# Performance work log

Hardware: AMD Instinct MI355X
Metric: run time of the kernel (lower is better)

The kernel has to match this reference:

```python
import jax, jax.numpy as jnp
import numpy as np

N = 100000      # num nodes
R = 32          # num relations
E = 3200000     # num edges
F_IN = 128      # feat_len
H = 16          # hidden dim (hard-coded in source)
C = 8           # num classes


def setup_inputs() -> dict:
    key = jax.random.key(0)
    k1, k2, k3, k4, k5 = jax.random.split(key, 5)
    emb = jax.random.normal(k1, (N, F_IN), dtype=jnp.float32)
    W1 = jax.random.normal(k2, (R, F_IN, H), dtype=jnp.float32) * 0.05
    W2 = jax.random.normal(k3, (R, H, C), dtype=jnp.float32) * 0.05
    edge_index = jax.random.randint(k4, (2, E), 0, N, dtype=jnp.int64)
    edge_type = jax.random.randint(k5, (E,), 0, R, dtype=jnp.int64)
    return {"emb": emb, "W1": W1, "W2": W2,
            "edge_index": edge_index, "edge_type": edge_type}


def _rgcn_layer(x, W, src, dst, etype, edge_norm):
    # x: [N, Fin], W: [R, Fin, Fout]
    # Transform once per relation, then gather per edge (avoids [E,Fin,Fout]).
    xw = jnp.einsum('nf,rfo->rno', x, W)          # [R, N, Fout]
    msg = xw[etype, src] * edge_norm[:, None]      # [E, Fout]
    return jax.ops.segment_sum(msg, dst, num_segments=N)  # [N, Fout]


def reference(emb, W1, W2, edge_index, edge_type):
    src, dst = edge_index[0], edge_index[1]
    # PyG RGCNConv aggr='mean': normalize by per-(dst, relation) in-degree.
    key_idx = dst * R + edge_type                              # [E]
    deg = jax.ops.segment_sum(jnp.ones((E,), emb.dtype), key_idx,
                              num_segments=N * R)              # [N*R]
    edge_norm = 1.0 / jnp.maximum(deg, 1.0)
    edge_norm = edge_norm[key_idx]                             # [E]

    h = jax.nn.relu(_rgcn_layer(emb, W1, src, dst, edge_type, edge_norm))
    h = _rgcn_layer(h, W2, src, dst, edge_type, edge_norm)
    return jax.nn.log_softmax(h, axis=1)
```

## Files before the change

### kernel.cpp

```cpp
#include <hip/hip_runtime.h>
#include <hip/hip_bf16.h>
#include <math.h>

#define N_NODES 100000
#define R 32
#define E_EDGES 3200000
#define F_IN 128
#define HDIM 16
#define CDIM 8
#define NOUT 512
#define M_PAD 100032
#define NBUCK 391
#define KEYS 8192
#define P1CHUNK 8192
#define P1GRID ((E_EDGES + P1CHUNK - 1) / P1CHUNK)

typedef __attribute__((ext_vector_type(8))) short bf16x8;
typedef __attribute__((ext_vector_type(4))) float f32x4;
typedef __attribute__((ext_vector_type(2))) _Float16 f16x2;

static __device__ __forceinline__ unsigned short f2bf(float f) {
    unsigned int u = __float_as_uint(f);
    unsigned int r = (u + 0x7FFFu + ((u >> 16) & 1u)) >> 16;
    return (unsigned short)r;
}
static __device__ __forceinline__ f16x2 asf16x2(float f) {
    union { float f; f16x2 h; } u; u.f = f; return u.h;
}

#if __has_builtin(__builtin_amdgcn_fdot2)
static __device__ __forceinline__ float FDOT2(f16x2 a, f16x2 b, float c) {
    return __builtin_amdgcn_fdot2(a, b, c, false);
}
#else
static __device__ __forceinline__ float FDOT2(f16x2 a, f16x2 b, float c) {
    return c + (float)a.x * (float)b.x + (float)a.y * (float)b.y;
}
#endif

__global__ __launch_bounds__(512) void k_hist(const int* __restrict__ dst,
                                              int* __restrict__ bucketcount) {
    __shared__ int h[NBUCK];
    int t = threadIdx.x;
    for (int j = t; j < NBUCK; j += 512) h[j] = 0;
    __syncthreads();
    int e0 = blockIdx.x * P1CHUNK;
    int e1 = e0 + P1CHUNK; if (e1 > E_EDGES) e1 = E_EDGES;
    int n4 = (e1 - e0) >> 2;
    const int4* d4 = (const int4*)(dst + e0);
    for (int i = t; i < n4; i += 512) {
        int4 v = d4[i];
        atomicAdd(&h[v.x >> 8], 1);
        atomicAdd(&h[v.y >> 8], 1);
        atomicAdd(&h[v.z >> 8], 1);
        atomicAdd(&h[v.w >> 8], 1);
    }
    __syncthreads();
    for (int j = t; j < NBUCK; j += 512)
        if (h[j]) atomicAdd(&bucketcount[j], h[j]);
}

__global__ __launch_bounds__(512) void k_scanb(const int* __restrict__ bucketcount,
                                               int* __restrict__ bucketstart,
                                               int* __restrict__ gcursor,
                                               int* __restrict__ rowstart) {
    __shared__ int sb[NBUCK + 1];
    int t = threadIdx.x;
    if (t == 0) {
        int acc = 0;
        for (int b = 0; b < NBUCK; ++b) { int v = bucketcount[b]; sb[b] = acc; acc += v; }
        sb[NBUCK] = acc;
        rowstart[N_NODES] = acc;
    }
    __syncthreads();
    for (int j = t; j <= NBUCK; j += 512) bucketstart[j] = sb[j];
    for (int j = t; j < NBUCK; j += 512) gcursor[j] = sb[j];
}

__global__ __launch_bounds__(512) void k_bucket(const int* __restrict__ src,
                                                const int* __restrict__ dst,
                                                const int* __restrict__ et,
                                                int* __restrict__ gcursor,
                                                unsigned int* __restrict__ ebuf) {
    __shared__ int hist[NBUCK];
    __shared__ int rank[NBUCK];
    __shared__ int base[NBUCK];
    int t = threadIdx.x;
    for (int j = t; j < NBUCK; j += 512) { hist[j] = 0; rank[j] = 0; }
    __syncthreads();
    int e0 = blockIdx.x * P1CHUNK;
    int e1 = e0 + P1CHUNK; if (e1 > E_EDGES) e1 = E_EDGES;
    int n4 = (e1 - e0) >> 2;
    const int4* d4 = (const int4*)(dst + e0);
    const int4* s4 = (const int4*)(src + e0);
    const int4* t4 = (const int4*)(et + e0);
    for (int i = t; i < n4; i += 512) {
        int4 v = d4[i];
        atomicAdd(&hist[v.x >> 8], 1);
        atomicAdd(&hist[v.y >> 8], 1);
        atomicAdd(&hist[v.z >> 8], 1);
        atomicAdd(&hist[v.w >> 8], 1);
    }
    __syncthreads();
    for (int j = t; j < NBUCK; j += 512)
        base[j] = hist[j] ? atomicAdd(&gcursor[j], hist[j]) : 0;
    __syncthreads();
    for (int i = t; i < n4; i += 512) {
        int4 dv = d4[i];
        int4 sv = s4[i];
        int4 tv = t4[i];
        int ds[4] = {dv.x, dv.y, dv.z, dv.w};
        int ss[4] = {sv.x, sv.y, sv.z, sv.w};
        int ts[4] = {tv.x, tv.y, tv.z, tv.w};
        #pragma unroll
        for (int u = 0; u < 4; ++u) {
            int d = ds[u];
            int bk = d >> 8;
            unsigned pk = ((unsigned)(d & 255) << 22) | ((unsigned)ts[u] << 17)
                        | (unsigned)ss[u];
            int lr = atomicAdd(&rank[bk], 1);
            ebuf[base[bk] + lr] = pk;
        }
    }
}

__global__ __launch_bounds__(1024) void k_sortb(const unsigned int* __restrict__ ebuf,
                                                const int* __restrict__ bucketstart,
                                                int* __restrict__ rowstart,
                                                unsigned int* __restrict__ elist) {
    __shared__ unsigned int cnt[KEYS];
    __shared__ int wsum[16];
    int t = threadIdx.x, b = blockIdx.x;
    int e0 = bucketstart[b], e1 = bucketstart[b + 1];
    #pragma unroll
    for (int j = 0; j < KEYS / 1024; ++j) cnt[t + j * 1024] = 0;
    __syncthreads();
    for (int i = e0 + t; i < e1; i += 1024)
        atomicAdd(&cnt[ebuf[i] >> 17], 1u);
    __syncthreads();
    int kbase = t * (KEYS / 1024);
    int s = 0;
    #pragma unroll
    for (int j = 0; j < KEYS / 1024; ++j) s += (int)cnt[kbase + j];
    int lane = t & 63, wv = t >> 6;
    int sc = s;
    #pragma unroll
    for (int off = 1; off < 64; off <<= 1) {
        int v = __shfl_up(sc, off, 64);
        if (lane >= off) sc += v;
    }
    if (lane == 63) wsum[wv] = sc;
    __syncthreads();
    if (t < 16) {
        int v = wsum[t];
        int sc2 = v;
        #pragma unroll
        for (int off = 1; off < 16; off <<= 1) {
            int u = __shfl_up(sc2, off, 16);
            if (t >= off) sc2 += u;
        }
        wsum[t] = sc2 - v;
    }
    __syncthreads();
    int run = wsum[wv] + sc - s;
    #pragma unroll
    for (int j = 0; j < KEYS / 1024; ++j) {
        unsigned v = cnt[kbase + j];
        unsigned lc = v > 1023u ? 1023u : v;
        cnt[kbase + j] = (unsigned)run | (lc << 20);
        run += (int)v;
    }
    __syncthreads();
    if (t < 256) {
        int d = b * 256 + t;
        if (d < N_NODES) rowstart[d] = e0 + (int)(cnt[t * 32] & 0xFFFFFu);
    }
    __syncthreads();
    for (int i = e0 + t; i < e1; i += 1024) {
        unsigned pk = ebuf[i];
        int key = pk >> 17;
        unsigned vv = atomicAdd(&cnt[key], 1u);
        int pos = (int)(vv & 0xFFFFFu);
        unsigned len = (vv >> 20) & 1023u;
        elist[e0 + pos] = (pk & 0x3FFFFFu) | (len << 22);
    }
}

__global__ __launch_bounds__(256) void k_cvt(const float* __restrict__ emb,
                                             unsigned short* __restrict__ out) {
    int g = blockIdx.x * 256 + threadIdx.x;
    size_t base = (size_t)g * 4;
    if (base >= (size_t)M_PAD * F_IN) return;
    int row = (int)(base >> 7);
    ushort4 o;
    if (row < N_NODES) {
        float4 a = *(const float4*)(emb + base);
        o.x = f2bf(a.x); o.y = f2bf(a.y); o.z = f2bf(a.z); o.w = f2bf(a.w);
    } else {
        o.x = o.y = o.z = o.w = 0;
    }
    *(ushort4*)(out + base) = o;
}

__global__ __launch_bounds__(256) void k_prep_w(const float* __restrict__ W1,
                                                unsigned short* __restrict__ BmT) {
    int i = blockIdx.x * 256 + threadIdx.x;
    if (i >= NOUT * F_IN) return;
    int n = i >> 7;
    int f = i & 127;
    int r = n >> 4;
    int o = n & 15;
    BmT[i] = f2bf(W1[r * (F_IN * HDIM) + f * HDIM + o]);
}

__global__ __launch_bounds__(256) void k_gemm(const unsigned short* __restrict__ Abf,
                                              const unsigned short* __restrict__ BmT,
                                              unsigned short* __restrict__ C) {
    __shared__ unsigned short As[64 * 136];
    __shared__ unsigned short Bs[128 * 136];
    int t = threadIdx.x;
    int row0 = blockIdx.x * 64;
    int col0 = blockIdx.y * 128;

    #pragma unroll
    for (int j = 0; j < 4; ++j) {
        int idx = t + j * 256;
        int r = idx >> 4;
        int u = idx & 15;
        float4 v = *(const float4*)(Abf + (size_t)(row0 + r) * F_IN + u * 8);
        *(float4*)(&As[r * 136 + u * 8]) = v;
    }
    #pragma unroll
    for (int j = 0; j < 8; ++j) {
        int idx = t + j * 256;
        int r = idx >> 4;
        int u = idx & 15;
        float4 v = *(const float4*)(BmT + (size_t)(col0 + r) * F_IN + u * 8);
        *(float4*)(&Bs[r * 136 + u * 8]) = v;
    }
    __syncthreads();

    int w = t >> 6;
    int lane = t & 63;
    int q = lane >> 4;
    int mr = lane & 15;

    f32x4 acc[8] = {};
    const unsigned short* ap = &As[(w * 16 + mr) * 136 + q * 8];
    #pragma unroll
    for (int kk = 0; kk < 4; ++kk) {
        bf16x8 af = *(const bf16x8*)(ap + kk * 32);
        #pragma unroll
        for (int tt = 0; tt < 8; ++tt) {
            bf16x8 bf = *(const bf16x8*)(&Bs[(tt * 16 + mr) * 136 + q * 8 + kk * 32]);
            acc[tt] = __builtin_amdgcn_mfma_f32_16x16x32_bf16(af, bf, acc[tt], 0, 0, 0);
        }
    }
    #pragma unroll
    for (int tt = 0; tt < 8; ++tt) {
        #pragma unroll
        for (int j = 0; j < 4; ++j) {
            int row = row0 + w * 16 + q * 4 + j;
            C[(size_t)row * NOUT + col0 + tt * 16 + mr] = f2bf(acc[tt][j]);
        }
    }
}

__global__ __launch_bounds__(256) void k_gather1(const int* __restrict__ rowstart,
                                                 const unsigned int* __restrict__ elist,
                                                 const unsigned short* __restrict__ xw1,
                                                 _Float16* __restrict__ h) {
    __shared__ float nlut[1024];
    int t = threadIdx.x;
    for (int j = t; j < 1024; j += 256) nlut[j] = 1.0f / (float)(j ? j : 1);
    __syncthreads();
    int g = t >> 3;
    int c = t & 7;
    int d = blockIdx.x * 32 + g;
    if (d >= N_NODES) return;
    int i = rowstart[d], end = rowstart[d + 1];
    float a0 = 0.f, a1 = 0.f, b0 = 0.f, b1 = 0.f;
    for (; i + 1 < end; i += 2) {
        unsigned pk0 = elist[i];
        unsigned pk1 = elist[i + 1];
        int s0 = pk0 & 0x1FFFF, s1 = pk1 & 0x1FFFF;
        int r0 = (pk0 >> 17) & 31, r1 = (pk1 >> 17) & 31;
        float nm0 = nlut[pk0 >> 22], nm1 = nlut[pk1 >> 22];
        unsigned x0 = *(const unsigned*)(xw1 + (size_t)s0 * NOUT + r0 * HDIM + c * 2);
        unsigned x1 = *(const unsigned*)(xw1 + (size_t)s1 * NOUT + r1 * HDIM + c * 2);
        a0 += __uint_as_float(x0 << 16) * nm0;
        a1 += __uint_as_float(x0 & 0xFFFF0000u) * nm0;
        b0 += __uint_as_float(x1 << 16) * nm1;
        b1 += __uint_as_float(x1 & 0xFFFF0000u) * nm1;
    }
    if (i < end) {
        unsigned pk = elist[i];
        int s = pk & 0x1FFFF;
        int r = (pk >> 17) & 31;
        float nm = nlut[pk >> 22];
        unsigned x = *(const unsigned*)(xw1 + (size_t)s * NOUT + r * HDIM + c * 2);
        a0 += __uint_as_float(x << 16) * nm;
        a1 += __uint_as_float(x & 0xFFFF0000u) * nm;
    }
    f16x2 o;
    o.x = (_Float16)fmaxf(a0 + b0, 0.f);
    o.y = (_Float16)fmaxf(a1 + b1, 0.f);
    *(f16x2*)(h + (size_t)d * HDIM + c * 2) = o;
}

#define W2P 260
__global__ __launch_bounds__(256) void k_gather2(const int* __restrict__ rowstart,
                                                 const unsigned int* __restrict__ elist,
                                                 const _Float16* __restrict__ h,
                                                 const float* __restrict__ W2,
                                                 float* __restrict__ out) {
    __shared__ f16x2 sW2h[CDIM * W2P];
    __shared__ float nlut[1024];
    int t = threadIdx.x;
    for (int j = t; j < 1024; j += 256) nlut[j] = 1.0f / (float)(j ? j : 1);
    #pragma unroll
    for (int j = 0; j < 8; ++j) {
        int idx = t + j * 256;
        int c = idx >> 8;
        int rem = idx & 255;
        int r = rem >> 3;
        int jj = rem & 7;
        f16x2 p;
        p.x = (_Float16)W2[r * (HDIM * CDIM) + (2 * jj) * CDIM + c];
        p.y = (_Float16)W2[r * (HDIM * CDIM) + (2 * jj + 1) * CDIM + c];
        sW2h[c * W2P + rem] = p;
    }
    __syncthreads();

    int g = t >> 3;
    int c = t & 7;
    int d = blockIdx.x * 32 + g;
    if (d >= N_NODES) return;
    const f16x2* wc = &sW2h[c * W2P];
    int i = rowstart[d], end = rowstart[d + 1];
    float acc0 = 0.f, acc1 = 0.f;
    for (; i + 1 < end; i += 2) {
        unsigned pk0 = elist[i];
        unsigned pk1 = elist[i + 1];
        int s0 = pk0 & 0x1FFFF, s1 = pk1 & 0x1FFFF;
        int r0 = (pk0 >> 17) & 31, r1 = (pk1 >> 17) & 31;
        float nm0 = nlut[pk0 >> 22], nm1 = nlut[pk1 >> 22];
        const float4* hp0 = (const float4*)(h + (size_t)s0 * HDIM);
        const float4* hp1 = (const float4*)(h + (size_t)s1 * HDIM);
        float4 u0 = hp0[0], u1 = hp0[1];
        float4 v0 = hp1[0], v1 = hp1[1];
        const f16x2* wp0 = wc + r0 * 8;
        const f16x2* wp1 = wc + r1 * 8;
        float sd0 = 0.f, sd1 = 0.f;
        sd0 = FDOT2(asf16x2(u0.x), wp0[0], sd0);
        sd0 = FDOT2(asf16x2(u0.y), wp0[1], sd0);
        sd0 = FDOT2(asf16x2(u0.z), wp0[2], sd0);
        sd0 = FDOT2(asf16x2(u0.w), wp0[3], sd0);
        sd0 = FDOT2(asf16x2(u1.x), wp0[4], sd0);
        sd0 = FDOT2(asf16x2(u1.y), wp0[5], sd0);
        sd0 = FDOT2(asf16x2(u1.z), wp0[6], sd0);
        sd0 = FDOT2(asf16x2(u1.w), wp0[7], sd0);
        sd1 = FDOT2(asf16x2(v0.x), wp1[0], sd1);
        sd1 = FDOT2(asf16x2(v0.y), wp1[1], sd1);
        sd1 = FDOT2(asf16x2(v0.z), wp1[2], sd1);
        sd1 = FDOT2(asf16x2(v0.w), wp1[3], sd1);
        sd1 = FDOT2(asf16x2(v1.x), wp1[4], sd1);
        sd1 = FDOT2(asf16x2(v1.y), wp1[5], sd1);
        sd1 = FDOT2(asf16x2(v1.z), wp1[6], sd1);
        sd1 = FDOT2(asf16x2(v1.w), wp1[7], sd1);
        acc0 += nm0 * sd0;
        acc1 += nm1 * sd1;
    }
    if (i < end) {
        unsigned pk = elist[i];
        int s = pk & 0x1FFFF;
        int r = (pk >> 17) & 31;
        float nm = nlut[pk >> 22];
        const float4* hp = (const float4*)(h + (size_t)s * HDIM);
        float4 u0 = hp[0], u1 = hp[1];
        const f16x2* wp = wc + r * 8;
        float sd = 0.f;
        sd = FDOT2(asf16x2(u0.x), wp[0], sd);
        sd = FDOT2(asf16x2(u0.y), wp[1], sd);
        sd = FDOT2(asf16x2(u0.z), wp[2], sd);
        sd = FDOT2(asf16x2(u0.w), wp[3], sd);
        sd = FDOT2(asf16x2(u1.x), wp[4], sd);
        sd = FDOT2(asf16x2(u1.y), wp[5], sd);
        sd = FDOT2(asf16x2(u1.z), wp[6], sd);
        sd = FDOT2(asf16x2(u1.w), wp[7], sd);
        acc0 += nm * sd;
    }
    float acc = acc0 + acc1;
    float m = acc;
    #pragma unroll
    for (int mask = 1; mask < 8; mask <<= 1)
        m = fmaxf(m, __shfl_xor(m, mask, 8));
    float ex = expf(acc - m);
    float ssumv = ex;
    #pragma unroll
    for (int mask = 1; mask < 8; mask <<= 1)
        ssumv += __shfl_xor(ssumv, mask, 8);
    out[(size_t)d * CDIM + c] = acc - m - logf(ssumv);
}

extern "C" void kernel_launch(void* const* d_in, const int* in_sizes, int n_in,
                              void* d_out, int out_size, void* d_ws, size_t ws_size,
                              hipStream_t stream) {
    const float* emb = (const float*)d_in[0];
    const float* W1  = (const float*)d_in[1];
    const float* W2  = (const float*)d_in[2];
    const int* ei    = (const int*)d_in[3];
    const int* et    = (const int*)d_in[4];
    const int* srcp  = ei;
    const int* dstp  = ei + E_EDGES;

    char* ws = (char*)d_ws;
    size_t off = 0;
    #define ALIGN256(x) (((x) + 255) & ~(size_t)255)
    int* bucketcount = (int*)(ws + off); off = ALIGN256(off + 512 * 4);
    int* bucketstart = (int*)(ws + off); off = ALIGN256(off + 512 * 4);
    int* gcursor     = (int*)(ws + off); off = ALIGN256(off + 512 * 4);
    int* rowstart    = (int*)(ws + off); off = ALIGN256(off + ((size_t)N_NODES + 8) * 4);
    unsigned int* ebuf  = (unsigned int*)(ws + off); off = ALIGN256(off + (size_t)E_EDGES * 4);
    unsigned int* elist = (unsigned int*)(ws + off); off = ALIGN256(off + (size_t)E_EDGES * 4);
    unsigned short* BmT  = (unsigned short*)(ws + off); off = ALIGN256(off + (size_t)NOUT * F_IN * 2);
    unsigned short* ebf  = (unsigned short*)(ws + off); off = ALIGN256(off + (size_t)M_PAD * F_IN * 2);
    unsigned short* xw1  = (unsigned short*)(ws + off); off = ALIGN256(off + (size_t)M_PAD * NOUT * 2);
    _Float16* h          = (_Float16*)(ws + off);       off = ALIGN256(off + (size_t)N_NODES * HDIM * 2);
    float* out = (float*)d_out;

    hipMemsetAsync(bucketcount, 0, NBUCK * 4, stream);

    k_hist<<<P1GRID, 512, 0, stream>>>(dstp, bucketcount);
    k_scanb<<<1, 512, 0, stream>>>(bucketcount, bucketstart, gcursor, rowstart);
    k_bucket<<<P1GRID, 512, 0, stream>>>(srcp, dstp, et, gcursor, ebuf);
    k_sortb<<<NBUCK, 1024, 0, stream>>>(ebuf, bucketstart, rowstart, elist);

    k_cvt<<<((M_PAD * F_IN / 4) + 255) / 256, 256, 0, stream>>>(emb, ebf);
    k_prep_w<<<(NOUT * F_IN) / 256, 256, 0, stream>>>(W1, BmT);
    dim3 g_gemm(M_PAD / 64, NOUT / 128);
    k_gemm<<<g_gemm, 256, 0, stream>>>(ebf, BmT, xw1);

    k_gather1<<<(N_NODES + 31) / 32, 256, 0, stream>>>(rowstart, elist, xw1, h);
    k_gather2<<<(N_NODES + 31) / 32, 256, 0, stream>>>(rowstart, elist, h, W2, out);
}
```

Baseline: 347.4 us.

## Merge preprocessing kernels via fixed-capacity buckets and widen gather1 per-thread loads

Bucketing now writes into fixed-capacity per-bucket slots (CAP 9216), so the separate histogram pass is gone. Bucketing, the bf16 conversion of emb and the W1 repack now run as one heterogeneous launch, and the per-bucket sort runs alongside the GEMM in a second combined launch, cutting launch count and the serialisation between them. gather1 now has each thread handle 4 features with 8-byte loads and unroll by 4 edges. The cost is a larger workspace, and results will be wrong if a bucket ever holds more than CAP edges. The combined kernels also force both roles to share one block size and one shared-memory allocation.

```diff
diff --git a/kernel.cpp b/kernel.cpp
--- a/kernel.cpp
+++ b/kernel.cpp
@@ -11,19 +11,31 @@
 #define NOUT 512
 #define M_PAD 100032
 #define NBUCK 391
+#define CAP 9216
 #define KEYS 8192
 #define P1CHUNK 8192
-#define P1GRID ((E_EDGES + P1CHUNK - 1) / P1CHUNK)
+#define CVT_BLKS 6252
+#define PREP_BLKS 128
+#define FRONT_GRID (NBUCK + CVT_BLKS + PREP_BLKS)
+#define GEMM_BLKS 6252
+#define MID_GRID (NBUCK + GEMM_BLKS)
 
 typedef __attribute__((ext_vector_type(8))) short bf16x8;
 typedef __attribute__((ext_vector_type(4))) float f32x4;
 typedef __attribute__((ext_vector_type(2))) _Float16 f16x2;
+typedef __attribute__((ext_vector_type(4))) _Float16 f16x4;
 
 static __device__ __forceinline__ unsigned short f2bf(float f) {
     unsigned int u = __float_as_uint(f);
     unsigned int r = (u + 0x7FFFu + ((u >> 16) & 1u)) >> 16;
     return (unsigned short)r;
 }
+static __device__ __forceinline__ float bfl(unsigned x) {
+    return __uint_as_float(x << 16);
+}
+static __device__ __forceinline__ float bfh(unsigned x) {
+    return __uint_as_float(x & 0xFFFF0000u);
+}
 static __device__ __forceinline__ f16x2 asf16x2(float f) {
     union { float f; f16x2 h; } u; u.f = f; return u.h;
 }
@@ -38,230 +50,201 @@
 }
 #endif
 
-__global__ __launch_bounds__(512) void k_hist(const int* __restrict__ dst,
-                                              int* __restrict__ bucketcount) {
-    __shared__ int h[NBUCK];
-    int t = threadIdx.x;
-    for (int j = t; j < NBUCK; j += 512) h[j] = 0;
-    __syncthreads();
-    int e0 = blockIdx.x * P1CHUNK;
-    int e1 = e0 + P1CHUNK; if (e1 > E_EDGES) e1 = E_EDGES;
-    int n4 = (e1 - e0) >> 2;
-    const int4* d4 = (const int4*)(dst + e0);
-    for (int i = t; i < n4; i += 512) {
-        int4 v = d4[i];
-        atomicAdd(&h[v.x >> 8], 1);
-        atomicAdd(&h[v.y >> 8], 1);
-        atomicAdd(&h[v.z >> 8], 1);
-        atomicAdd(&h[v.w >> 8], 1);
-    }
-    __syncthreads();
-    for (int j = t; j < NBUCK; j += 512)
-        if (h[j]) atomicAdd(&bucketcount[j], h[j]);
-}
-
-__global__ __launch_bounds__(512) void k_scanb(const int* __restrict__ bucketcount,
+__global__ __launch_bounds__(512) void k_front(const int* __restrict__ src,
+                                               const int* __restrict__ dst,
+                                               const int* __restrict__ et,
+                                               const float* __restrict__ emb,
+                                               const float* __restrict__ W1,
+                                               int* __restrict__ gcursor,
+                                               unsigned int* __restrict__ ebuf,
+                                               unsigned short* __restrict__ ebf,
+                                               unsigned short* __restrict__ BmT) {
+    __shared__ int sh[3 * NBUCK];
+    int b = blockIdx.x, t = threadIdx.x;
+    if (b < NBUCK) {
+        int* hist = sh;
+        int* rank = sh + NBUCK;
+        int* base = sh + 2 * NBUCK;
+        for (int j = t; j < NBUCK; j += 512) { hist[j] = 0; rank[j] = 0; }
+        __syncthreads();
+        int e0 = b * P1CHUNK;
+        int e1 = e0 + P1CHUNK; if (e1 > E_EDGES) e1 = E_EDGES;
+        int n4 = (e1 - e0) >> 2;
+        const int4* d4 = (const int4*)(dst + e0);
+        const int4* s4 = (const int4*)(src + e0);
+        const int4* t4 = (const int4*)(et + e0);
+        for (int i = t; i < n4; i += 512) {
+            int4 v = d4[i];
+            atomicAdd(&hist[v.x >> 8], 1);
+            atomicAdd(&hist[v.y >> 8], 1);
+            atomicAdd(&hist[v.z >> 8], 1);
+            atomicAdd(&hist[v.w >> 8], 1);
+        }
+        __syncthreads();
+        for (int j = t; j < NBUCK; j += 512)
+            base[j] = hist[j] ? atomicAdd(&gcursor[j], hist[j]) : 0;
+        __syncthreads();
+        for (int i = t; i < n4; i += 512) {
+            int4 dv = d4[i];
+            int4 sv = s4[i];
+            int4 tv = t4[i];
+            int ds[4] = {dv.x, dv.y, dv.z, dv.w};
+            int ss[4] = {sv.x, sv.y, sv.z, sv.w};
+            int ts[4] = {tv.x, tv.y, tv.z, tv.w};
+            #pragma unroll
+            for (int u = 0; u < 4; ++u) {
+                int d = ds[u];
+                int bk = d >> 8;
+                unsigned pk = ((unsigned)(d & 255) << 22) | ((unsigned)ts[u] << 17)
+                            | (unsigned)ss[u];
+                int lr = atomicAdd(&rank[bk], 1);
+                ebuf[(size_t)bk * CAP + base[bk] + lr] = pk;
+            }
+        }
+    } else if (b < NBUCK + CVT_BLKS) {
+        size_t base = ((size_t)(b - NBUCK) * 512 + t) * 4;
+        int row = (int)(base >> 7);
+        ushort4 o;
+        if (row < N_NODES) {
+            float4 a = *(const float4*)(emb + base);
+            o.x = f2bf(a.x); o.y = f2bf(a.y); o.z = f2bf(a.z); o.w = f2bf(a.w);
+        } else {
+            o.x = o.y = o.z = o.w = 0;
+        }
+        *(ushort4*)(ebf + base) = o;
+    } else {
+        int i = (b - NBUCK - CVT_BLKS) * 512 + t;
+        int n = i >> 7;
+        int f = i & 127;
+        int r = n >> 4;
+        int o = n & 15;
+        BmT[i] = f2bf(W1[r * (F_IN * HDIM) + f * HDIM + o]);
+    }
+}
+
+__global__ __launch_bounds__(512) void k_scanb(const int* __restrict__ gcursor,
                                                int* __restrict__ bucketstart,
-                                               int* __restrict__ gcursor,
                                                int* __restrict__ rowstart) {
     __shared__ int sb[NBUCK + 1];
     int t = threadIdx.x;
     if (t == 0) {
         int acc = 0;
-        for (int b = 0; b < NBUCK; ++b) { int v = bucketcount[b]; sb[b] = acc; acc += v; }
+        for (int b = 0; b < NBUCK; ++b) { int v = gcursor[b]; sb[b] = acc; acc += v; }
         sb[NBUCK] = acc;
         rowstart[N_NODES] = acc;
     }
     __syncthreads();
     for (int j = t; j <= NBUCK; j += 512) bucketstart[j] = sb[j];
-    for (int j = t; j < NBUCK; j += 512) gcursor[j] = sb[j];
-}
-
-__global__ __launch_bounds__(512) void k_bucket(const int* __restrict__ src,
-                                                const int* __restrict__ dst,
-                                                const int* __restrict__ et,
-                                                int* __restrict__ gcursor,
-                                                unsigned int* __restrict__ ebuf) {
-    __shared__ int hist[NBUCK];
-    __shared__ int rank[NBUCK];
-    __shared__ int base[NBUCK];
-    int t = threadIdx.x;
-    for (int j = t; j < NBUCK; j += 512) { hist[j] = 0; rank[j] = 0; }
-    __syncthreads();
-    int e0 = blockIdx.x * P1CHUNK;
-    int e1 = e0 + P1CHUNK; if (e1 > E_EDGES) e1 = E_EDGES;
-    int n4 = (e1 - e0) >> 2;
-    const int4* d4 = (const int4*)(dst + e0);
-    const int4* s4 = (const int4*)(src + e0);
-    const int4* t4 = (const int4*)(et + e0);
-    for (int i = t; i < n4; i += 512) {
-        int4 v = d4[i];
-        atomicAdd(&hist[v.x >> 8], 1);
-        atomicAdd(&hist[v.y >> 8], 1);
-        atomicAdd(&hist[v.z >> 8], 1);
-        atomicAdd(&hist[v.w >> 8], 1);
-    }
-    __syncthreads();
-    for (int j = t; j < NBUCK; j += 512)
-        base[j] = hist[j] ? atomicAdd(&gcursor[j], hist[j]) : 0;
-    __syncthreads();
-    for (int i = t; i < n4; i += 512) {
-        int4 dv = d4[i];
-        int4 sv = s4[i];
-        int4 tv = t4[i];
-        int ds[4] = {dv.x, dv.y, dv.z, dv.w};
-        int ss[4] = {sv.x, sv.y, sv.z, sv.w};
-        int ts[4] = {tv.x, tv.y, tv.z, tv.w};
-        #pragma unroll
-        for (int u = 0; u < 4; ++u) {
-            int d = ds[u];
-            int bk = d >> 8;
-            unsigned pk = ((unsigned)(d & 255) << 22) | ((unsigned)ts[u] << 17)
-                        | (unsigned)ss[u];
-            int lr = atomicAdd(&rank[bk], 1);
-            ebuf[base[bk] + lr] = pk;
-        }
-    }
-}
-
-__global__ __launch_bounds__(1024) void k_sortb(const unsigned int* __restrict__ ebuf,
-                                                const int* __restrict__ bucketstart,
-                                                int* __restrict__ rowstart,
-                                                unsigned int* __restrict__ elist) {
-    __shared__ unsigned int cnt[KEYS];
-    __shared__ int wsum[16];
-    int t = threadIdx.x, b = blockIdx.x;
-    int e0 = bucketstart[b], e1 = bucketstart[b + 1];
-    #pragma unroll
-    for (int j = 0; j < KEYS / 1024; ++j) cnt[t + j * 1024] = 0;
-    __syncthreads();
-    for (int i = e0 + t; i < e1; i += 1024)
-        atomicAdd(&cnt[ebuf[i] >> 17], 1u);
-    __syncthreads();
-    int kbase = t * (KEYS / 1024);
-    int s = 0;
-    #pragma unroll
-    for (int j = 0; j < KEYS / 1024; ++j) s += (int)cnt[kbase + j];
-    int lane = t & 63, wv = t >> 6;
-    int sc = s;
-    #pragma unroll
-    for (int off = 1; off < 64; off <<= 1) {
-        int v = __shfl_up(sc, off, 64);
-        if (lane >= off) sc += v;
-    }
-    if (lane == 63) wsum[wv] = sc;
-    __syncthreads();
-    if (t < 16) {
-        int v = wsum[t];
-        int sc2 = v;
-        #pragma unroll
-        for (int off = 1; off < 16; off <<= 1) {
-            int u = __shfl_up(sc2, off, 16);
-            if (t >= off) sc2 += u;
-        }
-        wsum[t] = sc2 - v;
-    }
-    __syncthreads();
-    int run = wsum[wv] + sc - s;
-    #pragma unroll
-    for (int j = 0; j < KEYS / 1024; ++j) {
-        unsigned v = cnt[kbase + j];
-        unsigned lc = v > 1023u ? 1023u : v;
-        cnt[kbase + j] = (unsigned)run | (lc << 20);
-        run += (int)v;
-    }
-    __syncthreads();
-    if (t < 256) {
-        int d = b * 256 + t;
-        if (d < N_NODES) rowstart[d] = e0 + (int)(cnt[t * 32] & 0xFFFFFu);
-    }
-    __syncthreads();
-    for (int i = e0 + t; i < e1; i += 1024) {
-        unsigned pk = ebuf[i];
-        int key = pk >> 17;
-        unsigned vv = atomicAdd(&cnt[key], 1u);
-        int pos = (int)(vv & 0xFFFFFu);
-        unsigned len = (vv >> 20) & 1023u;
-        elist[e0 + pos] = (pk & 0x3FFFFFu) | (len << 22);
-    }
-}
-
-__global__ __launch_bounds__(256) void k_cvt(const float* __restrict__ emb,
-                                             unsigned short* __restrict__ out) {
-    int g = blockIdx.x * 256 + threadIdx.x;
-    size_t base = (size_t)g * 4;
-    if (base >= (size_t)M_PAD * F_IN) return;
-    int row = (int)(base >> 7);
-    ushort4 o;
-    if (row < N_NODES) {
-        float4 a = *(const float4*)(emb + base);
-        o.x = f2bf(a.x); o.y = f2bf(a.y); o.z = f2bf(a.z); o.w = f2bf(a.w);
+}
+
+__global__ __launch_bounds__(256) void k_mid(const unsigned int* __restrict__ ebuf,
+                                             const int* __restrict__ gcursor,
+                                             const int* __restrict__ bucketstart,
+                                             int* __restrict__ rowstart,
+                                             unsigned int* __restrict__ elist,
+                                             const unsigned short* __restrict__ Abf,
+                                             const unsigned short* __restrict__ BmT,
+                                             unsigned short* __restrict__ C) {
+    __shared__ __align__(16) char smem[52224 + 64];
+    int b = blockIdx.x, t = threadIdx.x;
+    if (b < NBUCK) {
+        unsigned int* cnt = (unsigned int*)smem;
+        int* wsum = (int*)(smem + 32768);
+        int cntE = gcursor[b];
+        size_t esrc = (size_t)b * CAP;
+        int e0 = bucketstart[b];
+        #pragma unroll
+        for (int j = 0; j < KEYS / 256; ++j) cnt[t + j * 256] = 0;
+        __syncthreads();
+        for (int i = t; i < cntE; i += 256)
+            atomicAdd(&cnt[ebuf[esrc + i] >> 17], 1u);
+        __syncthreads();
+        int kbase = t * (KEYS / 256);
+        int s = 0;
+        #pragma unroll
+        for (int j = 0; j < KEYS / 256; ++j) s += (int)cnt[kbase + j];
+        int lane = t & 63, wv = t >> 6;
+        int sc = s;
+        #pragma unroll
+        for (int off = 1; off < 64; off <<= 1) {
+            int v = __shfl_up(sc, off, 64);
+            if (lane >= off) sc += v;
+        }
+        if (lane == 63) wsum[wv] = sc;
+        __syncthreads();
+        if (t == 0) {
+            int a = 0;
+            #pragma unroll
+            for (int w = 0; w < 4; ++w) { int v = wsum[w]; wsum[w] = a; a += v; }
+        }
+        __syncthreads();
+        int run = wsum[wv] + sc - s;
+        #pragma unroll
+        for (int j = 0; j < KEYS / 256; ++j) {
+            unsigned v = cnt[kbase + j];
+            unsigned lc = v > 1023u ? 1023u : v;
+            cnt[kbase + j] = (unsigned)run | (lc << 20);
+            run += (int)v;
+        }
+        __syncthreads();
+        {
+            int d = b * 256 + t;
+            if (d < N_NODES) rowstart[d] = e0 + (int)(cnt[t * 32] & 0xFFFFFu);
+        }
+        __syncthreads();
+        for (int i = t; i < cntE; i += 256) {
+            unsigned pk = ebuf[esrc + i];
+            int key = pk >> 17;
+            unsigned vv = atomicAdd(&cnt[key], 1u);
+            int pos = (int)(vv & 0xFFFFFu);
+            unsigned len = (vv >> 20) & 1023u;
+            elist[e0 + pos] = (pk & 0x3FFFFFu) | (len << 22);
+        }
     } else {
-        o.x = o.y = o.z = o.w = 0;
-    }
-    *(ushort4*)(out + base) = o;
-}
-
-__global__ __launch_bounds__(256) void k_prep_w(const float* __restrict__ W1,
-                                                unsigned short* __restrict__ BmT) {
-    int i = blockIdx.x * 256 + threadIdx.x;
-    if (i >= NOUT * F_IN) return;
-    int n = i >> 7;
-    int f = i & 127;
-    int r = n >> 4;
-    int o = n & 15;
-    BmT[i] = f2bf(W1[r * (F_IN * HDIM) + f * HDIM + o]);
-}
-
-__global__ __launch_bounds__(256) void k_gemm(const unsigned short* __restrict__ Abf,
-                                              const unsigned short* __restrict__ BmT,
-                                              unsigned short* __restrict__ C) {
-    __shared__ unsigned short As[64 * 136];
-    __shared__ unsigned short Bs[128 * 136];
-    int t = threadIdx.x;
-    int row0 = blockIdx.x * 64;
-    int col0 = blockIdx.y * 128;
-
-    #pragma unroll
-    for (int j = 0; j < 4; ++j) {
-        int idx = t + j * 256;
-        int r = idx >> 4;
-        int u = idx & 15;
-        float4 v = *(const float4*)(Abf + (size_t)(row0 + r) * F_IN + u * 8);
-        *(float4*)(&As[r * 136 + u * 8]) = v;
-    }
-    #pragma unroll
-    for (int j = 0; j < 8; ++j) {
-        int idx = t + j * 256;
-        int r = idx >> 4;
-        int u = idx & 15;
-        float4 v = *(const float4*)(BmT + (size_t)(col0 + r) * F_IN + u * 8);
-        *(float4*)(&Bs[r * 136 + u * 8]) = v;
-    }
-    __syncthreads();
-
-    int w = t >> 6;
-    int lane = t & 63;
-    int q = lane >> 4;
-    int mr = lane & 15;
-
-    f32x4 acc[8] = {};
-    const unsigned short* ap = &As[(w * 16 + mr) * 136 + q * 8];
-    #pragma unroll
-    for (int kk = 0; kk < 4; ++kk) {
-        bf16x8 af = *(const bf16x8*)(ap + kk * 32);
+        unsigned short* As = (unsigned short*)smem;
+        unsigned short* Bs = (unsigned short*)(smem + 17408);
+        int bb = b - NBUCK;
+        int row0 = (bb >> 2) * 64;
+        int col0 = (bb & 3) * 128;
+        #pragma unroll
+        for (int j = 0; j < 4; ++j) {
+            int idx = t + j * 256;
+            int r = idx >> 4;
+            int u = idx & 15;
+            float4 v = *(const float4*)(Abf + (size_t)(row0 + r) * F_IN + u * 8);
+            *(float4*)(&As[r * 136 + u * 8]) = v;
+        }
+        #pragma unroll
+        for (int j = 0; j < 8; ++j) {
+            int idx = t + j * 256;
+            int r = idx >> 4;
+            int u = idx & 15;
+            float4 v = *(const float4*)(BmT + (size_t)(col0 + r) * F_IN + u * 8);
+            *(float4*)(&Bs[r * 136 + u * 8]) = v;
+        }
+        __syncthreads();
+        int w = t >> 6;
+        int lane = t & 63;
+        int q = lane >> 4;
+        int mr = lane & 15;
+        f32x4 acc[8] = {};
+        const unsigned short* ap = &As[(w * 16 + mr) * 136 + q * 8];
+        #pragma unroll
+        for (int kk = 0; kk < 4; ++kk) {
+            bf16x8 af = *(const bf16x8*)(ap + kk * 32);
+            #pragma unroll
+            for (int tt = 0; tt < 8; ++tt) {
+                bf16x8 bf = *(const bf16x8*)(&Bs[(tt * 16 + mr) * 136 + q * 8 + kk * 32]);
+                acc[tt] = __builtin_amdgcn_mfma_f32_16x16x32_bf16(af, bf, acc[tt], 0, 0, 0);
+            }
+        }
         #pragma unroll
         for (int tt = 0; tt < 8; ++tt) {
-            bf16x8 bf = *(const bf16x8*)(&Bs[(tt * 16 + mr) * 136 + q * 8 + kk * 32]);
-            acc[tt] = __builtin_amdgcn_mfma_f32_16x16x32_bf16(af, bf, acc[tt], 0, 0, 0);
-        }
-    }
-    #pragma unroll
-    for (int tt = 0; tt < 8; ++tt) {
-        #pragma unroll
-        for (int j = 0; j < 4; ++j) {
-            int row = row0 + w * 16 + q * 4 + j;
-            C[(size_t)row * NOUT + col0 + tt * 16 + mr] = f2bf(acc[tt][j]);
+            #pragma unroll
+            for (int j = 0; j < 4; ++j) {
+                int row = row0 + w * 16 + q * 4 + j;
+                C[(size_t)row * NOUT + col0 + tt * 16 + mr] = f2bf(acc[tt][j]);
+            }
         }
     }
 }
@@ -274,38 +257,40 @@
     int t = threadIdx.x;
     for (int j = t; j < 1024; j += 256) nlut[j] = 1.0f / (float)(j ? j : 1);
     __syncthreads();
-    int g = t >> 3;
-    int c = t & 7;
-    int d = blockIdx.x * 32 + g;
+    int g = t >> 2;
+    int c = t & 3;
+    int d = blockIdx.x * 64 + g;
     if (d >= N_NODES) return;
     int i = rowstart[d], end = rowstart[d + 1];
-    float a0 = 0.f, a1 = 0.f, b0 = 0.f, b1 = 0.f;
-    for (; i + 1 < end; i += 2) {
+    float a0 = 0.f, a1 = 0.f, a2 = 0.f, a3 = 0.f;
+    for (; i + 3 < end; i += 4) {
         unsigned pk0 = elist[i];
         unsigned pk1 = elist[i + 1];
-        int s0 = pk0 & 0x1FFFF, s1 = pk1 & 0x1FFFF;
-        int r0 = (pk0 >> 17) & 31, r1 = (pk1 >> 17) & 31;
-        float nm0 = nlut[pk0 >> 22], nm1 = nlut[pk1 >> 22];
-        unsigned x0 = *(const unsigned*)(xw1 + (size_t)s0 * NOUT + r0 * HDIM + c * 2);
-        unsigned x1 = *(const unsigned*)(xw1 + (size_t)s1 * NOUT + r1 * HDIM + c * 2);
-        a0 += __uint_as_float(x0 << 16) * nm0;
-        a1 += __uint_as_float(x0 & 0xFFFF0000u) * nm0;
-        b0 += __uint_as_float(x1 << 16) * nm1;
-        b1 += __uint_as_float(x1 & 0xFFFF0000u) * nm1;
-    }
-    if (i < end) {
+        unsigned pk2 = elist[i + 2];
+        unsigned pk3 = elist[i + 3];
+        uint2 x0 = *(const uint2*)(xw1 + (size_t)(pk0 & 0x1FFFF) * NOUT + ((pk0 >> 17) & 31) * HDIM + c * 4);
+        uint2 x1 = *(const uint2*)(xw1 + (size_t)(pk1 & 0x1FFFF) * NOUT + ((pk1 >> 17) & 31) * HDIM + c * 4);
+        uint2 x2 = *(const uint2*)(xw1 + (size_t)(pk2 & 0x1FFFF) * NOUT + ((pk2 >> 17) & 31) * HDIM + c * 4);
+        uint2 x3 = *(const uint2*)(xw1 + (size_t)(pk3 & 0x1FFFF) * NOUT + ((pk3 >> 17) & 31) * HDIM + c * 4);
+        float n0 = nlut[pk0 >> 22], n1 = nlut[pk1 >> 22];
+        float n2 = nlut[pk2 >> 22], n3 = nlut[pk3 >> 22];
+        a0 += bfl(x0.x) * n0; a1 += bfh(x0.x) * n0; a2 += bfl(x0.y) * n0; a3 += bfh(x0.y) * n0;
+        a0 += bfl(x1.x) * n1; a1 += bfh(x1.x) * n1; a2 += bfl(x1.y) * n1; a3 += bfh(x1.y) * n1;
+        a0 += bfl(x2.x) * n2; a1 += bfh(x2.x) * n2; a2 += bfl(x2.y) * n2; a3 += bfh(x2.y) * n2;
+        a0 += bfl(x3.x) * n3; a1 += bfh(x3.x) * n3; a2 += bfl(x3.y) * n3; a3 += bfh(x3.y) * n3;
+    }
+    for (; i < end; ++i) {
         unsigned pk = elist[i];
-        int s = pk & 0x1FFFF;
-        int r = (pk >> 17) & 31;
+        uint2 x = *(const uint2*)(xw1 + (size_t)(pk & 0x1FFFF) * NOUT + ((pk >> 17) & 31) * HDIM + c * 4);
         float nm = nlut[pk >> 22];
-        unsigned x = *(const unsigned*)(xw1 + (size_t)s * NOUT + r * HDIM + c * 2);
-        a0 += __uint_as_float(x << 16) * nm;
-        a1 += __uint_as_float(x & 0xFFFF0000u) * nm;
-    }
-    f16x2 o;
-    o.x = (_Float16)fmaxf(a0 + b0, 0.f);
-    o.y = (_Float16)fmaxf(a1 + b1, 0.f);
-    *(f16x2*)(h + (size_t)d * HDIM + c * 2) = o;
+        a0 += bfl(x.x) * nm; a1 += bfh(x.x) * nm; a2 += bfl(x.y) * nm; a3 += bfh(x.y) * nm;
+    }
+    f16x4 o;
+    o.x = (_Float16)fmaxf(a0, 0.f);
+    o.y = (_Float16)fmaxf(a1, 0.f);
+    o.z = (_Float16)fmaxf(a2, 0.f);
+    o.w = (_Float16)fmaxf(a3, 0.f);
+    *(f16x4*)(h + (size_t)d * HDIM + c * 4) = o;
 }
 
 #define W2P 260
@@ -342,15 +327,13 @@
     for (; i + 1 < end; i += 2) {
         unsigned pk0 = elist[i];
         unsigned pk1 = elist[i + 1];
-        int s0 = pk0 & 0x1FFFF, s1 = pk1 & 0x1FFFF;
-        int r0 = (pk0 >> 17) & 31, r1 = (pk1 >> 17) & 31;
-        float nm0 = nlut[pk0 >> 22], nm1 = nlut[pk1 >> 22];
-        const float4* hp0 = (const float4*)(h + (size_t)s0 * HDIM);
-        const float4* hp1 = (const float4*)(h + (size_t)s1 * HDIM);
+        const float4* hp0 = (const float4*)(h + (size_t)(pk0 & 0x1FFFF) * HDIM);
+        const float4* hp1 = (const float4*)(h + (size_t)(pk1 & 0x1FFFF) * HDIM);
         float4 u0 = hp0[0], u1 = hp0[1];
         float4 v0 = hp1[0], v1 = hp1[1];
-        const f16x2* wp0 = wc + r0 * 8;
-        const f16x2* wp1 = wc + r1 * 8;
+        float nm0 = nlut[pk0 >> 22], nm1 = nlut[pk1 >> 22];
+        const f16x2* wp0 = wc + ((pk0 >> 17) & 31) * 8;
+        const f16x2* wp1 = wc + ((pk1 >> 17) & 31) * 8;
         float sd0 = 0.f, sd1 = 0.f;
         sd0 = FDOT2(asf16x2(u0.x), wp0[0], sd0);
         sd0 = FDOT2(asf16x2(u0.y), wp0[1], sd0);
@@ -373,12 +356,10 @@
     }
     if (i < end) {
         unsigned pk = elist[i];
-        int s = pk & 0x1FFFF;
-        int r = (pk >> 17) & 31;
+        const float4* hp = (const float4*)(h + (size_t)(pk & 0x1FFFF) * HDIM);
+        float4 u0 = hp[0], u1 = hp[1];
         float nm = nlut[pk >> 22];
-        const float4* hp = (const float4*)(h + (size_t)s * HDIM);
-        float4 u0 = hp[0], u1 = hp[1];
-        const f16x2* wp = wc + r * 8;
+        const f16x2* wp = wc + ((pk >> 17) & 31) * 8;
         float sd = 0.f;
         sd = FDOT2(asf16x2(u0.x), wp[0], sd);
         sd = FDOT2(asf16x2(u0.y), wp[1], sd);
@@ -417,11 +398,10 @@
     char* ws = (char*)d_ws;
     size_t off = 0;
     #define ALIGN256(x) (((x) + 255) & ~(size_t)255)
-    int* bucketcount = (int*)(ws + off); off = ALIGN256(off + 512 * 4);
+    int* gcursor     = (int*)(ws + off); off = ALIGN256(off + 512 * 4);
     int* bucketstart = (int*)(ws + off); off = ALIGN256(off + 512 * 4);
-    int* gcursor     = (int*)(ws + off); off = ALIGN256(off + 512 * 4);
     int* rowstart    = (int*)(ws + off); off = ALIGN256(off + ((size_t)N_NODES + 8) * 4);
-    unsigned int* ebuf  = (unsigned int*)(ws + off); off = ALIGN256(off + (size_t)E_EDGES * 4);
+    unsigned int* ebuf  = (unsigned int*)(ws + off); off = ALIGN256(off + (size_t)NBUCK * CAP * 4);
     unsigned int* elist = (unsigned int*)(ws + off); off = ALIGN256(off + (size_t)E_EDGES * 4);
     unsigned short* BmT  = (unsigned short*)(ws + off); off = ALIGN256(off + (size_t)NOUT * F_IN * 2);
     unsigned short* ebf  = (unsigned short*)(ws + off); off = ALIGN256(off + (size_t)M_PAD * F_IN * 2);
@@ -429,18 +409,11 @@
     _Float16* h          = (_Float16*)(ws + off);       off = ALIGN256(off + (size_t)N_NODES * HDIM * 2);
     float* out = (float*)d_out;
 
-    hipMemsetAsync(bucketcount, 0, NBUCK * 4, stream);
-
-    k_hist<<<P1GRID, 512, 0, stream>>>(dstp, bucketcount);
-    k_scanb<<<1, 512, 0, stream>>>(bucketcount, bucketstart, gcursor, rowstart);
-    k_bucket<<<P1GRID, 512, 0, stream>>>(srcp, dstp, et, gcursor, ebuf);
-    k_sortb<<<NBUCK, 1024, 0, stream>>>(ebuf, bucketstart, rowstart, elist);
-
-    k_cvt<<<((M_PAD * F_IN / 4) + 255) / 256, 256, 0, stream>>>(emb, ebf);
-    k_prep_w<<<(NOUT * F_IN) / 256, 256, 0, stream>>>(W1, BmT);
-    dim3 g_gemm(M_PAD / 64, NOUT / 128);
-    k_gemm<<<g_gemm, 256, 0, stream>>>(ebf, BmT, xw1);
-
-    k_gather1<<<(N_NODES + 31) / 32, 256, 0, stream>>>(rowstart, elist, xw1, h);
+    hipMemsetAsync(gcursor, 0, 512 * 4, stream);
+
+    k_front<<<FRONT_GRID, 512, 0, stream>>>(srcp, dstp, et, emb, W1, gcursor, ebuf, ebf, BmT);
+    k_scanb<<<1, 512, 0, stream>>>(gcursor, bucketstart, rowstart);
+    k_mid<<<MID_GRID, 256, 0, stream>>>(ebuf, gcursor, bucketstart, rowstart, elist, ebf, BmT, xw1);
+    k_gather1<<<(N_NODES + 63) / 64, 256, 0, stream>>>(rowstart, elist, xw1, h);
     k_gather2<<<(N_NODES + 31) / 32, 256, 0, stream>>>(rowstart, elist, h, W2, out);
 }
```

Measured after the change: 332.6 us. 4.3% less time.
